# Kernel optimization log

Measured on AMD Instinct MI355X. Metric: run time of the kernel, lower is better.

Reference implementation:

```python
import jax, jax.numpy as jnp
import numpy as np

N_NODES = 50000
N_EDGES = 800000
D = 128
N_GRAPHS = 64


def setup_inputs() -> dict:
    key = jax.random.key(0)
    ks = jax.random.split(key, 9)
    x = jax.random.normal(ks[0], (N_NODES, D), dtype=jnp.float32)
    edge_index = jax.random.randint(ks[1], (2, N_EDGES), 0, N_NODES, dtype=jnp.int32)
    batch = jnp.sort(jax.random.randint(ks[2], (N_NODES,), 0, N_GRAPHS, dtype=jnp.int32))
    s = 1.0 / np.sqrt(D)
    W1 = jax.random.normal(ks[3], (D, D), jnp.float32) * s
    W2 = jax.random.normal(ks[4], (D, D), jnp.float32) * s
    W3 = jax.random.normal(ks[5], (D, D), jnp.float32) * s
    b1 = jnp.zeros((D,), jnp.float32)
    b2 = jnp.zeros((D,), jnp.float32)
    b3 = jnp.zeros((D,), jnp.float32)
    return {"x": x, "W1": W1, "b1": b1, "W2": W2, "b2": b2, "W3": W3, "b3": b3,
            "edge_index": edge_index, "batch": batch}


def _gcn_conv(x, W, b, src, dst, deg_inv_sqrt):
    # PyG GCNConv: x' = D^{-1/2} (A+I) D^{-1/2} (x W) + b
    h = x @ W                                    # [N, D]
    norm = (deg_inv_sqrt[src] * deg_inv_sqrt[dst])[:, None]   # [E, 1]
    agg = jax.ops.segment_sum(h[src] * norm, dst, num_segments=N_NODES)
    # self-loop contribution: norm_ii = deg_i^{-1}
    agg = agg + (deg_inv_sqrt * deg_inv_sqrt)[:, None] * h
    return agg + b


def reference(x, W1, b1, W2, b2, W3, b3, edge_index, batch):
    src, dst = edge_index[0], edge_index[1]
    # degree on A + I (self-loops added), edge weight 1
    deg = jax.ops.segment_sum(jnp.ones((N_EDGES,), x.dtype), dst,
                              num_segments=N_NODES) + 1.0
    deg_inv_sqrt = jax.lax.rsqrt(deg)
    h = jax.nn.relu(_gcn_conv(x, W1, b1, src, dst, deg_inv_sqrt))
    h = jax.nn.relu(_gcn_conv(h, W2, b2, src, dst, deg_inv_sqrt))
    h = _gcn_conv(h, W3, b3, src, dst, deg_inv_sqrt)
    # global_max_pool over graph ids
    return jax.ops.segment_max(h, batch, num_segments=N_GRAPHS)
```

## Files before the change

### kernel.cpp

```cpp
#include <hip/hip_runtime.h>
#include <float.h>
#include <math.h>

#define D 128
#define PCHUNK 64
#define NBUCK 256
#define BROWS 196
#define BCAP 4096
#define ACHUNK 3125

typedef _Float16 half8 __attribute__((ext_vector_type(8)));
typedef _Float16 half2v __attribute__((ext_vector_type(2)));
typedef float f32x4 __attribute__((ext_vector_type(4)));

__device__ __forceinline__ unsigned encf(float x) {
    unsigned u = __float_as_uint(x);
    return (u & 0x80000000u) ? ~u : (u | 0x80000000u);
}
__device__ __forceinline__ float decf(unsigned e) {
    unsigned u = (e & 0x80000000u) ? (e & 0x7FFFFFFFu) : ~e;
    return __uint_as_float(u);
}

__global__ __launch_bounds__(256) void binA_kernel(const int* __restrict__ src,
                                                   const int* __restrict__ dst,
                                                   int* __restrict__ gcnt,
                                                   uint2* __restrict__ gpair, int ne) {
    __shared__ int lh[NBUCK], ssc[NBUCK], lstart[NBUCK], gbase[NBUCK], loff[NBUCK];
    __shared__ uint2 stage[ACHUNK + 8];
    int t = threadIdx.x;
    int e0 = blockIdx.x * ACHUNK;
    int e1 = min(e0 + ACHUNK, ne);
    lh[t] = 0;
    __syncthreads();
    for (int e = e0 + t; e < e1; e += 256) atomicAdd(&lh[dst[e] / BROWS], 1);
    __syncthreads();
    ssc[t] = lh[t];
    __syncthreads();
    for (int off = 1; off < NBUCK; off <<= 1) {
        int u = (t >= off) ? ssc[t - off] : 0;
        __syncthreads();
        ssc[t] += u;
        __syncthreads();
    }
    int st = ssc[t] - lh[t];
    lstart[t] = st;
    loff[t] = st;
    if (lh[t] > 0) gbase[t] = atomicAdd(&gcnt[t], lh[t]);
    __syncthreads();
    for (int e = e0 + t; e < e1; e += 256) {
        int s = src[e], d = dst[e];
        int pos = atomicAdd(&loff[d / BROWS], 1);
        stage[pos] = make_uint2((unsigned)s, (unsigned)d);
    }
    __syncthreads();
    int m = e1 - e0;
    for (int i = t; i < m; i += 256) {
        uint2 pr = stage[i];
        int b = (int)pr.y / BROWS;
        int gpos = b * BCAP + gbase[b] + (i - lstart[b]);
        if (gpos < (b + 1) * BCAP) gpair[gpos] = pr;
    }
}

__global__ __launch_bounds__(256) void binB_kernel(const uint2* __restrict__ gpair,
                                                   const int* __restrict__ gcnt,
                                                   int* __restrict__ rowptr,
                                                   float* __restrict__ disv,
                                                   int* __restrict__ csr, int n) {
    __shared__ int lh[256], ssc[256], lstart[256], loff[256];
    __shared__ int gsc[NBUCK];
    __shared__ int cstage[BCAP];
    int b = blockIdx.x, t = threadIdx.x;
    int myc = gcnt[t];
    gsc[t] = myc;
    __syncthreads();
    for (int off = 1; off < NBUCK; off <<= 1) {
        int u = (t >= off) ? gsc[t - off] : 0;
        __syncthreads();
        gsc[t] += u;
        __syncthreads();
    }
    int bs = gsc[b] - gcnt[b];
    int m = min(gcnt[b], BCAP);
    int row0 = b * BROWS;
    int nrows = min(BROWS, n - row0);
    if (nrows <= 0) return;
    const uint2* mp = gpair + (size_t)b * BCAP;
    lh[t] = 0;
    __syncthreads();
    for (int i = t; i < m; i += 256) atomicAdd(&lh[(int)mp[i].y - row0], 1);
    __syncthreads();
    ssc[t] = lh[t];
    __syncthreads();
    for (int off = 1; off < 256; off <<= 1) {
        int u = (t >= off) ? ssc[t - off] : 0;
        __syncthreads();
        ssc[t] += u;
        __syncthreads();
    }
    int st = ssc[t] - lh[t];
    lstart[t] = st;
    loff[t] = st;
    __syncthreads();
    if (t <= nrows) rowptr[row0 + t] = bs + lstart[t];
    if (t < nrows) disv[row0 + t] = rsqrtf((float)lh[t] + 1.0f);
    for (int i = t; i < m; i += 256) {
        uint2 pr = mp[i];
        int pos = atomicAdd(&loff[(int)pr.y - row0], 1);
        cstage[pos] = (int)pr.x;
    }
    __syncthreads();
    for (int i = t; i < m; i += 256) csr[bs + i] = cstage[i];
}

__global__ void pack3_kernel(const float* __restrict__ W1, const float* __restrict__ W2,
                             const float* __restrict__ W3, _Float16* __restrict__ Wp1,
                             _Float16* __restrict__ Wp2, _Float16* __restrict__ Wp3,
                             unsigned* __restrict__ outEnc, int nout) {
    int gi = blockIdx.x * blockDim.x + threadIdx.x;
    if (gi < nout) outEnc[gi] = 0x007FFFFFu;
    int w = gi >> 14, i = gi & 16383;
    const float* W = (w == 0) ? W1 : (w == 1) ? W2 : W3;
    _Float16* Wp = (w == 0) ? Wp1 : (w == 1) ? Wp2 : Wp3;
    int j = i & 7, l = (i >> 3) & 63, t = (i >> 9) & 7, s = (i >> 12) & 3;
    int k = s * 32 + ((l >> 4) << 3) + j;
    int c = t * 16 + (l & 15);
    Wp[i] = (_Float16)W[k * 128 + c];
}

template <bool F32SRC>
__global__ __launch_bounds__(256) void gemm_mfma(const void* __restrict__ Xsrc,
                                                 const _Float16* __restrict__ Wp,
                                                 const float* __restrict__ disv,
                                                 _Float16* __restrict__ Gh,
                                                 int ntiles, int n) {
    __shared__ _Float16 Wl[16384];
    int tid = threadIdx.x;
    {
        const uint4* s4 = (const uint4*)Wp;
        uint4* d4 = (uint4*)Wl;
#pragma unroll
        for (int i = 0; i < 8; i++) d4[tid + 256 * i] = s4[tid + 256 * i];
    }
    __syncthreads();
    int wave = tid >> 6, lane = tid & 63;
    int m = lane & 15, quad = lane >> 4;
    const half8* wfrag = (const half8*)Wl;
    const _Float16* Xh = (const _Float16*)Xsrc;
    const float* Xf = (const float*)Xsrc;

    int tile = blockIdx.x * 4 + wave;
    if (tile >= ntiles) return;
    int arow = tile * 16 + m;
    if (arow >= n) arow = n - 1;

    f32x4 acc[8];
#pragma unroll
    for (int t = 0; t < 8; t++) acc[t] = (f32x4){0.f, 0.f, 0.f, 0.f};

#pragma unroll
    for (int s = 0; s < 4; s++) {
        half8 a;
        if (F32SRC) {
            float4 lo = *(const float4*)(Xf + (size_t)arow * D + s * 32 + quad * 8);
            float4 hi = *(const float4*)(Xf + (size_t)arow * D + s * 32 + quad * 8 + 4);
            a[0] = (_Float16)lo.x; a[1] = (_Float16)lo.y; a[2] = (_Float16)lo.z; a[3] = (_Float16)lo.w;
            a[4] = (_Float16)hi.x; a[5] = (_Float16)hi.y; a[6] = (_Float16)hi.z; a[7] = (_Float16)hi.w;
        } else {
            a = *(const half8*)(Xh + (size_t)arow * D + s * 32 + quad * 8);
        }
#pragma unroll
        for (int t = 0; t < 8; t++) {
            half8 b = wfrag[(s * 8 + t) * 64 + lane];
            acc[t] = __builtin_amdgcn_mfma_f32_16x16x32_f16(a, b, acc[t], 0, 0, 0);
        }
    }
    int orow0 = tile * 16 + quad * 4;
    if (orow0 + 3 < n) {
        float d0 = disv[orow0], d1 = disv[orow0 + 1], d2 = disv[orow0 + 2], d3 = disv[orow0 + 3];
#pragma unroll
        for (int t = 0; t < 8; t++) {
            int col = t * 16 + m;
            Gh[(size_t)(orow0 + 0) * D + col] = (_Float16)(acc[t][0] * d0);
            Gh[(size_t)(orow0 + 1) * D + col] = (_Float16)(acc[t][1] * d1);
            Gh[(size_t)(orow0 + 2) * D + col] = (_Float16)(acc[t][2] * d2);
            Gh[(size_t)(orow0 + 3) * D + col] = (_Float16)(acc[t][3] * d3);
        }
    } else {
#pragma unroll
        for (int t = 0; t < 8; t++) {
            int col = t * 16 + m;
#pragma unroll
            for (int r = 0; r < 4; r++) {
                int orow = orow0 + r;
                if (orow < n) Gh[(size_t)orow * D + col] = (_Float16)(acc[t][r] * disv[orow]);
            }
        }
    }
}

__global__ __launch_bounds__(256) void agg_f16(const _Float16* __restrict__ G,
                                               const int* __restrict__ rowptr,
                                               const int* __restrict__ csr,
                                               const float* __restrict__ disv,
                                               const float* __restrict__ bias,
                                               _Float16* __restrict__ Out, int n, int relu) {
    int wave = threadIdx.x >> 6, lane = threadIdx.x & 63;
    int node = blockIdx.x * 4 + wave;
    if (node >= n) return;
    int sub = lane >> 4, li = lane & 15;
    const half8* G8 = (const half8*)G;
    float acc[8];
    if (sub == 0) {
        half8 sv = G8[(size_t)node * 16 + li];
#pragma unroll
        for (int j = 0; j < 8; j++) acc[j] = (float)sv[j];
    } else {
#pragma unroll
        for (int j = 0; j < 8; j++) acc[j] = 0.f;
    }
    int e = rowptr[node], end = rowptr[node + 1];
    for (; e + 16 <= end; e += 16) {
        int i0 = csr[e + sub], i1 = csr[e + 4 + sub];
        int i2 = csr[e + 8 + sub], i3 = csr[e + 12 + sub];
        half8 v0 = G8[(size_t)i0 * 16 + li];
        half8 v1 = G8[(size_t)i1 * 16 + li];
        half8 v2 = G8[(size_t)i2 * 16 + li];
        half8 v3 = G8[(size_t)i3 * 16 + li];
#pragma unroll
        for (int j = 0; j < 8; j++)
            acc[j] += ((float)v0[j] + (float)v1[j]) + ((float)v2[j] + (float)v3[j]);
    }
    for (; e + 4 <= end; e += 4) {
        int i0 = csr[e + sub];
        half8 v0 = G8[(size_t)i0 * 16 + li];
#pragma unroll
        for (int j = 0; j < 8; j++) acc[j] += (float)v0[j];
    }
    int r = end - e;
    if (sub < r) {
        int i0 = csr[e + sub];
        half8 v0 = G8[(size_t)i0 * 16 + li];
#pragma unroll
        for (int j = 0; j < 8; j++) acc[j] += (float)v0[j];
    }
#pragma unroll
    for (int j = 0; j < 8; j++) {
        acc[j] += __shfl_xor(acc[j], 16);
        acc[j] += __shfl_xor(acc[j], 32);
    }
    if (sub == 0) {
        float dd = disv[node];
        float4 b0 = *(const float4*)&bias[li * 8];
        float4 b1 = *(const float4*)&bias[li * 8 + 4];
        float o0 = fmaf(dd, acc[0], b0.x), o1 = fmaf(dd, acc[1], b0.y);
        float o2 = fmaf(dd, acc[2], b0.z), o3 = fmaf(dd, acc[3], b0.w);
        float o4 = fmaf(dd, acc[4], b1.x), o5 = fmaf(dd, acc[5], b1.y);
        float o6 = fmaf(dd, acc[6], b1.z), o7 = fmaf(dd, acc[7], b1.w);
        if (relu) {
            o0 = fmaxf(o0, 0.f); o1 = fmaxf(o1, 0.f); o2 = fmaxf(o2, 0.f); o3 = fmaxf(o3, 0.f);
            o4 = fmaxf(o4, 0.f); o5 = fmaxf(o5, 0.f); o6 = fmaxf(o6, 0.f); o7 = fmaxf(o7, 0.f);
        }
        half8 h;
        h[0] = (_Float16)o0; h[1] = (_Float16)o1; h[2] = (_Float16)o2; h[3] = (_Float16)o3;
        h[4] = (_Float16)o4; h[5] = (_Float16)o5; h[6] = (_Float16)o6; h[7] = (_Float16)o7;
        ((half8*)Out)[(size_t)node * 16 + li] = h;
    }
}

__global__ __launch_bounds__(128) void pool_kernel(const _Float16* __restrict__ H,
                                                   const int* __restrict__ batch,
                                                   unsigned* __restrict__ outEnc, int n) {
    int half = threadIdx.x >> 6;
    int li = threadIdx.x & 63;
    int start = blockIdx.x * PCHUNK + half * (PCHUNK / 2);
    if (start >= n) return;
    int end = min(start + PCHUNK / 2, n);
    int c = li * 2;
    int curg = batch[start];
    float cx = -INFINITY, cy = -INFINITY;
    for (int i = start; i < end; i++) {
        half2v v = *(const half2v*)(H + (size_t)i * D + c);
        float vx = (float)v[0], vy = (float)v[1];
        int g = batch[i];
        if (g != curg) {
            atomicMax(&outEnc[curg * D + c], encf(cx));
            atomicMax(&outEnc[curg * D + c + 1], encf(cy));
            cx = vx; cy = vy; curg = g;
        } else {
            cx = fmaxf(cx, vx); cy = fmaxf(cy, vy);
        }
    }
    atomicMax(&outEnc[curg * D + c], encf(cx));
    atomicMax(&outEnc[curg * D + c + 1], encf(cy));
}

__global__ void decode_kernel(const unsigned* __restrict__ outEnc, float* __restrict__ out, int n) {
    int i = blockIdx.x * blockDim.x + threadIdx.x;
    if (i < n) out[i] = decf(outEnc[i]);
}

extern "C" void kernel_launch(void* const* d_in, const int* in_sizes, int n_in,
                              void* d_out, int out_size, void* d_ws, size_t ws_size,
                              hipStream_t stream) {
    const float* x  = (const float*)d_in[0];
    const float* W1 = (const float*)d_in[1];
    const float* b1 = (const float*)d_in[2];
    const float* W2 = (const float*)d_in[3];
    const float* b2 = (const float*)d_in[4];
    const float* W3 = (const float*)d_in[5];
    const float* b3 = (const float*)d_in[6];
    const int* ei    = (const int*)d_in[7];
    const int* batch = (const int*)d_in[8];

    int n  = in_sizes[0] / D;
    int ne = in_sizes[7] / 2;
    const int* src = ei;
    const int* dst = ei + ne;

    char* p = (char*)d_ws;
    auto alloc = [&](size_t bytes) -> void* {
        void* q = (void*)p;
        p += (bytes + 255) & ~(size_t)255;
        return q;
    };
    _Float16* Gh  = (_Float16*)alloc((size_t)n * D * 2);
    _Float16* Hh  = (_Float16*)alloc((size_t)n * D * 2);
    _Float16* Wp1 = (_Float16*)alloc((size_t)D * D * 2);
    _Float16* Wp2 = (_Float16*)alloc((size_t)D * D * 2);
    _Float16* Wp3 = (_Float16*)alloc((size_t)D * D * 2);
    int* gcnt     = (int*)alloc((size_t)NBUCK * 4);
    uint2* gpair  = (uint2*)alloc((size_t)NBUCK * BCAP * 8);
    int* rowptr   = (int*)alloc((size_t)(n + 1) * 4);
    int* csr      = (int*)alloc((size_t)ne * 4);
    float* disv   = (float*)alloc((size_t)n * 4);
    unsigned* outEnc = (unsigned*)alloc((size_t)out_size * 4);

    hipMemsetAsync(gcnt, 0, (size_t)NBUCK * 4, stream);

    int nblocksA = (ne + ACHUNK - 1) / ACHUNK;
    binA_kernel<<<nblocksA, 256, 0, stream>>>(src, dst, gcnt, gpair, ne);
    binB_kernel<<<NBUCK, 256, 0, stream>>>(gpair, gcnt, rowptr, disv, csr, n);
    pack3_kernel<<<192, 256, 0, stream>>>(W1, W2, W3, Wp1, Wp2, Wp3, outEnc, out_size);

    int ntiles = (n + 15) / 16;
    int gemm_blocks = (ntiles + 3) / 4;
    int agg_blocks  = (n + 3) / 4;

    gemm_mfma<true><<<gemm_blocks, 256, 0, stream>>>(x, Wp1, disv, Gh, ntiles, n);
    agg_f16<<<agg_blocks, 256, 0, stream>>>(Gh, rowptr, csr, disv, b1, Hh, n, 1);
    gemm_mfma<false><<<gemm_blocks, 256, 0, stream>>>(Hh, Wp2, disv, Gh, ntiles, n);
    agg_f16<<<agg_blocks, 256, 0, stream>>>(Gh, rowptr, csr, disv, b2, Hh, n, 1);
    gemm_mfma<false><<<gemm_blocks, 256, 0, stream>>>(Hh, Wp3, disv, Gh, ntiles, n);
    agg_f16<<<agg_blocks, 256, 0, stream>>>(Gh, rowptr, csr, disv, b3, Hh, n, 0);

    pool_kernel<<<(n + PCHUNK - 1) / PCHUNK, 128, 0, stream>>>(Hh, batch, outEnc, n);
    decode_kernel<<<(out_size + 255) / 256, 256, 0, stream>>>(outEnc, (float*)d_out, out_size);
}
```

Before: 259.1 us.

## Split features into 32-column chunks so the gather working set fits in cache

Stores the GEMM output and hidden features in a chunked layout of four 32-column planes, each [N,32]. Aggregation now runs one block group per chunk, with 4 nodes per wave and 4 edge streams per node. Each gather pass therefore only touches a 3.2MB plane, which should improve L2 hit rates for the random neighbour reads. The cost is that the CSR indices are read four times and each gather is a smaller 64B row segment. Index loads and output stores also become nontemporal.

```diff
diff --git a/kernel.cpp b/kernel.cpp
--- a/kernel.cpp
+++ b/kernel.cpp
@@ -3,6 +3,8 @@
 #include <math.h>
 
 #define D 128
+#define NCHUNK 4
+#define CHW 32
 #define PCHUNK 64
 #define NBUCK 256
 #define BROWS 196
@@ -168,7 +170,7 @@
             a[0] = (_Float16)lo.x; a[1] = (_Float16)lo.y; a[2] = (_Float16)lo.z; a[3] = (_Float16)lo.w;
             a[4] = (_Float16)hi.x; a[5] = (_Float16)hi.y; a[6] = (_Float16)hi.z; a[7] = (_Float16)hi.w;
         } else {
-            a = *(const half8*)(Xh + (size_t)arow * D + s * 32 + quad * 8);
+            a = *(const half8*)(Xh + ((size_t)s * n + arow) * CHW + quad * 8);
         }
 #pragma unroll
         for (int t = 0; t < 8; t++) {
@@ -181,79 +183,87 @@
         float d0 = disv[orow0], d1 = disv[orow0 + 1], d2 = disv[orow0 + 2], d3 = disv[orow0 + 3];
 #pragma unroll
         for (int t = 0; t < 8; t++) {
-            int col = t * 16 + m;
-            Gh[(size_t)(orow0 + 0) * D + col] = (_Float16)(acc[t][0] * d0);
-            Gh[(size_t)(orow0 + 1) * D + col] = (_Float16)(acc[t][1] * d1);
-            Gh[(size_t)(orow0 + 2) * D + col] = (_Float16)(acc[t][2] * d2);
-            Gh[(size_t)(orow0 + 3) * D + col] = (_Float16)(acc[t][3] * d3);
+            int col = (t & 1) * 16 + m;
+            size_t rb = (size_t)(t >> 1) * n;
+            Gh[(rb + orow0 + 0) * CHW + col] = (_Float16)(acc[t][0] * d0);
+            Gh[(rb + orow0 + 1) * CHW + col] = (_Float16)(acc[t][1] * d1);
+            Gh[(rb + orow0 + 2) * CHW + col] = (_Float16)(acc[t][2] * d2);
+            Gh[(rb + orow0 + 3) * CHW + col] = (_Float16)(acc[t][3] * d3);
         }
     } else {
 #pragma unroll
         for (int t = 0; t < 8; t++) {
-            int col = t * 16 + m;
+            int col = (t & 1) * 16 + m;
+            size_t rb = (size_t)(t >> 1) * n;
 #pragma unroll
             for (int r = 0; r < 4; r++) {
                 int orow = orow0 + r;
-                if (orow < n) Gh[(size_t)orow * D + col] = (_Float16)(acc[t][r] * disv[orow]);
+                if (orow < n) Gh[(rb + orow) * CHW + col] = (_Float16)(acc[t][r] * disv[orow]);
             }
         }
     }
 }
 
-__global__ __launch_bounds__(256) void agg_f16(const _Float16* __restrict__ G,
-                                               const int* __restrict__ rowptr,
-                                               const int* __restrict__ csr,
-                                               const float* __restrict__ disv,
-                                               const float* __restrict__ bias,
-                                               _Float16* __restrict__ Out, int n, int relu) {
+__global__ __launch_bounds__(256) void agg_chunk(const _Float16* __restrict__ G,
+                                                 const int* __restrict__ rowptr,
+                                                 const int* __restrict__ csr,
+                                                 const float* __restrict__ disv,
+                                                 const float* __restrict__ bias,
+                                                 _Float16* __restrict__ Out, int n, int relu,
+                                                 int nodeblocks) {
+    int chunk = blockIdx.x / nodeblocks;
+    int nb = blockIdx.x - chunk * nodeblocks;
     int wave = threadIdx.x >> 6, lane = threadIdx.x & 63;
-    int node = blockIdx.x * 4 + wave;
-    if (node >= n) return;
-    int sub = lane >> 4, li = lane & 15;
+    int node = nb * 16 + wave * 4 + (lane >> 4);
+    if (node >= n) node = n - 1;
+    int stream = (lane >> 2) & 3, li = lane & 3;
     const half8* G8 = (const half8*)G;
+    size_t cb4 = (size_t)chunk * n * 4;
+
     float acc[8];
-    if (sub == 0) {
-        half8 sv = G8[(size_t)node * 16 + li];
+    if (stream == 0) {
+        half8 sv = G8[cb4 + (size_t)node * 4 + li];
 #pragma unroll
         for (int j = 0; j < 8; j++) acc[j] = (float)sv[j];
     } else {
 #pragma unroll
         for (int j = 0; j < 8; j++) acc[j] = 0.f;
     }
-    int e = rowptr[node], end = rowptr[node + 1];
-    for (; e + 16 <= end; e += 16) {
-        int i0 = csr[e + sub], i1 = csr[e + 4 + sub];
-        int i2 = csr[e + 8 + sub], i3 = csr[e + 12 + sub];
-        half8 v0 = G8[(size_t)i0 * 16 + li];
-        half8 v1 = G8[(size_t)i1 * 16 + li];
-        half8 v2 = G8[(size_t)i2 * 16 + li];
-        half8 v3 = G8[(size_t)i3 * 16 + li];
-#pragma unroll
-        for (int j = 0; j < 8; j++)
-            acc[j] += ((float)v0[j] + (float)v1[j]) + ((float)v2[j] + (float)v3[j]);
-    }
-    for (; e + 4 <= end; e += 4) {
-        int i0 = csr[e + sub];
-        half8 v0 = G8[(size_t)i0 * 16 + li];
-#pragma unroll
-        for (int j = 0; j < 8; j++) acc[j] += (float)v0[j];
-    }
-    int r = end - e;
-    if (sub < r) {
-        int i0 = csr[e + sub];
-        half8 v0 = G8[(size_t)i0 * 16 + li];
-#pragma unroll
-        for (int j = 0; j < 8; j++) acc[j] += (float)v0[j];
+
+    int rs = rowptr[node], re = rowptr[node + 1];
+    for (int eb = rs + stream * 4; eb < re; eb += 16) {
+        int cnt = re - eb;
+        if (cnt >= 4) {
+            int i0 = __builtin_nontemporal_load(csr + eb);
+            int i1 = __builtin_nontemporal_load(csr + eb + 1);
+            int i2 = __builtin_nontemporal_load(csr + eb + 2);
+            int i3 = __builtin_nontemporal_load(csr + eb + 3);
+            half8 v0 = G8[cb4 + (size_t)i0 * 4 + li];
+            half8 v1 = G8[cb4 + (size_t)i1 * 4 + li];
+            half8 v2 = G8[cb4 + (size_t)i2 * 4 + li];
+            half8 v3 = G8[cb4 + (size_t)i3 * 4 + li];
+#pragma unroll
+            for (int j = 0; j < 8; j++)
+                acc[j] += ((float)v0[j] + (float)v1[j]) + ((float)v2[j] + (float)v3[j]);
+        } else {
+            for (int k = 0; k < cnt; k++) {
+                int i0 = __builtin_nontemporal_load(csr + eb + k);
+                half8 v = G8[cb4 + (size_t)i0 * 4 + li];
+#pragma unroll
+                for (int j = 0; j < 8; j++) acc[j] += (float)v[j];
+            }
+        }
     }
 #pragma unroll
     for (int j = 0; j < 8; j++) {
-        acc[j] += __shfl_xor(acc[j], 16);
-        acc[j] += __shfl_xor(acc[j], 32);
-    }
-    if (sub == 0) {
+        acc[j] += __shfl_xor(acc[j], 4);
+        acc[j] += __shfl_xor(acc[j], 8);
+    }
+    if (stream == 0) {
         float dd = disv[node];
-        float4 b0 = *(const float4*)&bias[li * 8];
-        float4 b1 = *(const float4*)&bias[li * 8 + 4];
+        int col0 = chunk * CHW + li * 8;
+        float4 b0 = *(const float4*)&bias[col0];
+        float4 b1 = *(const float4*)&bias[col0 + 4];
         float o0 = fmaf(dd, acc[0], b0.x), o1 = fmaf(dd, acc[1], b0.y);
         float o2 = fmaf(dd, acc[2], b0.z), o3 = fmaf(dd, acc[3], b0.w);
         float o4 = fmaf(dd, acc[4], b1.x), o5 = fmaf(dd, acc[5], b1.y);
@@ -265,7 +275,7 @@
         half8 h;
         h[0] = (_Float16)o0; h[1] = (_Float16)o1; h[2] = (_Float16)o2; h[3] = (_Float16)o3;
         h[4] = (_Float16)o4; h[5] = (_Float16)o5; h[6] = (_Float16)o6; h[7] = (_Float16)o7;
-        ((half8*)Out)[(size_t)node * 16 + li] = h;
+        __builtin_nontemporal_store(h, (half8*)Out + cb4 + (size_t)node * 4 + li);
     }
 }
 
@@ -278,10 +288,13 @@
     if (start >= n) return;
     int end = min(start + PCHUNK / 2, n);
     int c = li * 2;
+    int chnk = c >> 5;
+    int off = c & 31;
+    const _Float16* Hc = H + (size_t)chnk * n * CHW + off;
     int curg = batch[start];
     float cx = -INFINITY, cy = -INFINITY;
     for (int i = start; i < end; i++) {
-        half2v v = *(const half2v*)(H + (size_t)i * D + c);
+        half2v v = *(const half2v*)(Hc + (size_t)i * CHW);
         float vx = (float)v[0], vy = (float)v[1];
         int g = batch[i];
         if (g != curg) {
@@ -346,14 +359,15 @@
 
     int ntiles = (n + 15) / 16;
     int gemm_blocks = (ntiles + 3) / 4;
-    int agg_blocks  = (n + 3) / 4;
+    int nodeblocks = (n + 15) / 16;
+    int agg_blocks = NCHUNK * nodeblocks;
 
     gemm_mfma<true><<<gemm_blocks, 256, 0, stream>>>(x, Wp1, disv, Gh, ntiles, n);
-    agg_f16<<<agg_blocks, 256, 0, stream>>>(Gh, rowptr, csr, disv, b1, Hh, n, 1);
+    agg_chunk<<<agg_blocks, 256, 0, stream>>>(Gh, rowptr, csr, disv, b1, Hh, n, 1, nodeblocks);
     gemm_mfma<false><<<gemm_blocks, 256, 0, stream>>>(Hh, Wp2, disv, Gh, ntiles, n);
-    agg_f16<<<agg_blocks, 256, 0, stream>>>(Gh, rowptr, csr, disv, b2, Hh, n, 1);
+    agg_chunk<<<agg_blocks, 256, 0, stream>>>(Gh, rowptr, csr, disv, b2, Hh, n, 1, nodeblocks);
     gemm_mfma<false><<<gemm_blocks, 256, 0, stream>>>(Hh, Wp3, disv, Gh, ntiles, n);
-    agg_f16<<<agg_blocks, 256, 0, stream>>>(Gh, rowptr, csr, disv, b3, Hh, n, 0);
+    agg_chunk<<<agg_blocks, 256, 0, stream>>>(Gh, rowptr, csr, disv, b3, Hh, n, 0, nodeblocks);
 
     pool_kernel<<<(n + PCHUNK - 1) / PCHUNK, 128, 0, stream>>>(Hh, batch, outEnc, n);
     decode_kernel<<<(out_size + 255) / 256, 256, 0, stream>>>(outEnc, (float*)d_out, out_size);
```

After: 328.6 us. +26.8%, slower.

## Pad CSR rows to multiples of four with per-bucket layout and vectorized index loads

Applied to the files above, without the earlier changes.

binB now places each bucket's CSR segment at a fixed per-bucket offset, which drops the global prefix scan over bucket counts. Each row's neighbor list is padded to a multiple of four using self-indices, and rowptr becomes an (offset, degree) pair. The aggregation kernel removes the padding contribution by scaling the self term by (1 - npad). This lets it use int4/int2 vectorized index loads and a simpler tail with no partial-row branch. The GEMM kernel now handles two tiles per block. The cost is some extra gathers of padding entries and a larger CSR buffer.

```diff
diff --git a/kernel.cpp b/kernel.cpp
--- a/kernel.cpp
+++ b/kernel.cpp
@@ -7,6 +7,7 @@
 #define NBUCK 256
 #define BROWS 196
 #define BCAP 4096
+#define BCAPP 4896
 #define ACHUNK 3125
 
 typedef _Float16 half8 __attribute__((ext_vector_type(8)));
@@ -65,23 +66,12 @@
 
 __global__ __launch_bounds__(256) void binB_kernel(const uint2* __restrict__ gpair,
                                                    const int* __restrict__ gcnt,
-                                                   int* __restrict__ rowptr,
+                                                   int2* __restrict__ rowptr2,
                                                    float* __restrict__ disv,
                                                    int* __restrict__ csr, int n) {
-    __shared__ int lh[256], ssc[256], lstart[256], loff[256];
-    __shared__ int gsc[NBUCK];
-    __shared__ int cstage[BCAP];
+    __shared__ int lh[256], ssc[256], loff[256];
+    __shared__ int cstage[BCAPP];
     int b = blockIdx.x, t = threadIdx.x;
-    int myc = gcnt[t];
-    gsc[t] = myc;
-    __syncthreads();
-    for (int off = 1; off < NBUCK; off <<= 1) {
-        int u = (t >= off) ? gsc[t - off] : 0;
-        __syncthreads();
-        gsc[t] += u;
-        __syncthreads();
-    }
-    int bs = gsc[b] - gcnt[b];
     int m = min(gcnt[b], BCAP);
     int row0 = b * BROWS;
     int nrows = min(BROWS, n - row0);
@@ -91,7 +81,9 @@
     __syncthreads();
     for (int i = t; i < m; i += 256) atomicAdd(&lh[(int)mp[i].y - row0], 1);
     __syncthreads();
-    ssc[t] = lh[t];
+    int deg = lh[t];
+    int pdeg = (deg + 3) & ~3;
+    ssc[t] = pdeg;
     __syncthreads();
     for (int off = 1; off < 256; off <<= 1) {
         int u = (t >= off) ? ssc[t - off] : 0;
@@ -99,19 +91,25 @@
         ssc[t] += u;
         __syncthreads();
     }
-    int st = ssc[t] - lh[t];
-    lstart[t] = st;
+    int st = ssc[t] - pdeg;
     loff[t] = st;
     __syncthreads();
-    if (t <= nrows) rowptr[row0 + t] = bs + lstart[t];
-    if (t < nrows) disv[row0 + t] = rsqrtf((float)lh[t] + 1.0f);
+    int bbase = b * BCAPP;
+    if (t < nrows) {
+        rowptr2[row0 + t] = make_int2(bbase + st, deg);
+        disv[row0 + t] = rsqrtf((float)deg + 1.0f);
+    }
     for (int i = t; i < m; i += 256) {
         uint2 pr = mp[i];
         int pos = atomicAdd(&loff[(int)pr.y - row0], 1);
         cstage[pos] = (int)pr.x;
     }
-    __syncthreads();
-    for (int i = t; i < m; i += 256) csr[bs + i] = cstage[i];
+    if (t < nrows) {
+        for (int k = deg; k < pdeg; k++) cstage[st + k] = row0 + t;
+    }
+    __syncthreads();
+    int ptot = ssc[255];
+    for (int i = t; i < ptot; i += 256) csr[bbase + i] = cstage[i];
 }
 
 __global__ void pack3_kernel(const float* __restrict__ W1, const float* __restrict__ W2,
@@ -150,58 +148,61 @@
     const _Float16* Xh = (const _Float16*)Xsrc;
     const float* Xf = (const float*)Xsrc;
 
-    int tile = blockIdx.x * 4 + wave;
-    if (tile >= ntiles) return;
-    int arow = tile * 16 + m;
-    if (arow >= n) arow = n - 1;
-
-    f32x4 acc[8];
-#pragma unroll
-    for (int t = 0; t < 8; t++) acc[t] = (f32x4){0.f, 0.f, 0.f, 0.f};
-
-#pragma unroll
-    for (int s = 0; s < 4; s++) {
-        half8 a;
-        if (F32SRC) {
-            float4 lo = *(const float4*)(Xf + (size_t)arow * D + s * 32 + quad * 8);
-            float4 hi = *(const float4*)(Xf + (size_t)arow * D + s * 32 + quad * 8 + 4);
-            a[0] = (_Float16)lo.x; a[1] = (_Float16)lo.y; a[2] = (_Float16)lo.z; a[3] = (_Float16)lo.w;
-            a[4] = (_Float16)hi.x; a[5] = (_Float16)hi.y; a[6] = (_Float16)hi.z; a[7] = (_Float16)hi.w;
-        } else {
-            a = *(const half8*)(Xh + (size_t)arow * D + s * 32 + quad * 8);
-        }
-#pragma unroll
-        for (int t = 0; t < 8; t++) {
-            half8 b = wfrag[(s * 8 + t) * 64 + lane];
-            acc[t] = __builtin_amdgcn_mfma_f32_16x16x32_f16(a, b, acc[t], 0, 0, 0);
-        }
-    }
-    int orow0 = tile * 16 + quad * 4;
-    if (orow0 + 3 < n) {
-        float d0 = disv[orow0], d1 = disv[orow0 + 1], d2 = disv[orow0 + 2], d3 = disv[orow0 + 3];
-#pragma unroll
-        for (int t = 0; t < 8; t++) {
-            int col = t * 16 + m;
-            Gh[(size_t)(orow0 + 0) * D + col] = (_Float16)(acc[t][0] * d0);
-            Gh[(size_t)(orow0 + 1) * D + col] = (_Float16)(acc[t][1] * d1);
-            Gh[(size_t)(orow0 + 2) * D + col] = (_Float16)(acc[t][2] * d2);
-            Gh[(size_t)(orow0 + 3) * D + col] = (_Float16)(acc[t][3] * d3);
-        }
-    } else {
-#pragma unroll
-        for (int t = 0; t < 8; t++) {
-            int col = t * 16 + m;
-#pragma unroll
-            for (int r = 0; r < 4; r++) {
-                int orow = orow0 + r;
-                if (orow < n) Gh[(size_t)orow * D + col] = (_Float16)(acc[t][r] * disv[orow]);
+#pragma unroll
+    for (int pass = 0; pass < 2; pass++) {
+        int tile = blockIdx.x * 8 + pass * 4 + wave;
+        if (tile >= ntiles) continue;
+        int arow = tile * 16 + m;
+        if (arow >= n) arow = n - 1;
+
+        f32x4 acc[8];
+#pragma unroll
+        for (int t = 0; t < 8; t++) acc[t] = (f32x4){0.f, 0.f, 0.f, 0.f};
+
+#pragma unroll
+        for (int s = 0; s < 4; s++) {
+            half8 a;
+            if (F32SRC) {
+                float4 lo = *(const float4*)(Xf + (size_t)arow * D + s * 32 + quad * 8);
+                float4 hi = *(const float4*)(Xf + (size_t)arow * D + s * 32 + quad * 8 + 4);
+                a[0] = (_Float16)lo.x; a[1] = (_Float16)lo.y; a[2] = (_Float16)lo.z; a[3] = (_Float16)lo.w;
+                a[4] = (_Float16)hi.x; a[5] = (_Float16)hi.y; a[6] = (_Float16)hi.z; a[7] = (_Float16)hi.w;
+            } else {
+                a = *(const half8*)(Xh + (size_t)arow * D + s * 32 + quad * 8);
+            }
+#pragma unroll
+            for (int t = 0; t < 8; t++) {
+                half8 bf = wfrag[(s * 8 + t) * 64 + lane];
+                acc[t] = __builtin_amdgcn_mfma_f32_16x16x32_f16(a, bf, acc[t], 0, 0, 0);
             }
         }
+        int orow0 = tile * 16 + quad * 4;
+        if (orow0 + 3 < n) {
+            float d0 = disv[orow0], d1 = disv[orow0 + 1], d2 = disv[orow0 + 2], d3 = disv[orow0 + 3];
+#pragma unroll
+            for (int t = 0; t < 8; t++) {
+                int col = t * 16 + m;
+                Gh[(size_t)(orow0 + 0) * D + col] = (_Float16)(acc[t][0] * d0);
+                Gh[(size_t)(orow0 + 1) * D + col] = (_Float16)(acc[t][1] * d1);
+                Gh[(size_t)(orow0 + 2) * D + col] = (_Float16)(acc[t][2] * d2);
+                Gh[(size_t)(orow0 + 3) * D + col] = (_Float16)(acc[t][3] * d3);
+            }
+        } else {
+#pragma unroll
+            for (int t = 0; t < 8; t++) {
+                int col = t * 16 + m;
+#pragma unroll
+                for (int r = 0; r < 4; r++) {
+                    int orow = orow0 + r;
+                    if (orow < n) Gh[(size_t)orow * D + col] = (_Float16)(acc[t][r] * disv[orow]);
+                }
+            }
+        }
     }
 }
 
 __global__ __launch_bounds__(256) void agg_f16(const _Float16* __restrict__ G,
-                                               const int* __restrict__ rowptr,
+                                               const int2* __restrict__ rowptr2,
                                                const int* __restrict__ csr,
                                                const float* __restrict__ disv,
                                                const float* __restrict__ bias,
@@ -211,35 +212,40 @@
     if (node >= n) return;
     int sub = lane >> 4, li = lane & 15;
     const half8* G8 = (const half8*)G;
+    int2 rp = rowptr2[node];
+    int e0 = rp.x, deg = rp.y;
+    int pend = e0 + ((deg + 3) & ~3);
+    int npad = pend - e0 - deg;
     float acc[8];
     if (sub == 0) {
         half8 sv = G8[(size_t)node * 16 + li];
-#pragma unroll
-        for (int j = 0; j < 8; j++) acc[j] = (float)sv[j];
+        float w = (float)(1 - npad);
+#pragma unroll
+        for (int j = 0; j < 8; j++) acc[j] = w * (float)sv[j];
     } else {
 #pragma unroll
         for (int j = 0; j < 8; j++) acc[j] = 0.f;
     }
-    int e = rowptr[node], end = rowptr[node + 1];
-    for (; e + 16 <= end; e += 16) {
-        int i0 = csr[e + sub], i1 = csr[e + 4 + sub];
-        int i2 = csr[e + 8 + sub], i3 = csr[e + 12 + sub];
-        half8 v0 = G8[(size_t)i0 * 16 + li];
-        half8 v1 = G8[(size_t)i1 * 16 + li];
-        half8 v2 = G8[(size_t)i2 * 16 + li];
-        half8 v3 = G8[(size_t)i3 * 16 + li];
+    int e = e0;
+    for (; e + 16 <= pend; e += 16) {
+        int4 ix = *(const int4*)(csr + e + sub * 4);
+        half8 v0 = G8[(size_t)ix.x * 16 + li];
+        half8 v1 = G8[(size_t)ix.y * 16 + li];
+        half8 v2 = G8[(size_t)ix.z * 16 + li];
+        half8 v3 = G8[(size_t)ix.w * 16 + li];
 #pragma unroll
         for (int j = 0; j < 8; j++)
             acc[j] += ((float)v0[j] + (float)v1[j]) + ((float)v2[j] + (float)v3[j]);
     }
-    for (; e + 4 <= end; e += 4) {
-        int i0 = csr[e + sub];
-        half8 v0 = G8[(size_t)i0 * 16 + li];
-#pragma unroll
-        for (int j = 0; j < 8; j++) acc[j] += (float)v0[j];
-    }
-    int r = end - e;
-    if (sub < r) {
+    if (e + 8 <= pend) {
+        int2 ix = *(const int2*)(csr + e + sub * 2);
+        half8 v0 = G8[(size_t)ix.x * 16 + li];
+        half8 v1 = G8[(size_t)ix.y * 16 + li];
+#pragma unroll
+        for (int j = 0; j < 8; j++) acc[j] += (float)v0[j] + (float)v1[j];
+        e += 8;
+    }
+    if (e < pend) {
         int i0 = csr[e + sub];
         half8 v0 = G8[(size_t)i0 * 16 + li];
 #pragma unroll
@@ -332,8 +338,8 @@
     _Float16* Wp3 = (_Float16*)alloc((size_t)D * D * 2);
     int* gcnt     = (int*)alloc((size_t)NBUCK * 4);
     uint2* gpair  = (uint2*)alloc((size_t)NBUCK * BCAP * 8);
-    int* rowptr   = (int*)alloc((size_t)(n + 1) * 4);
-    int* csr      = (int*)alloc((size_t)ne * 4);
+    int2* rowptr2 = (int2*)alloc((size_t)n * 8);
+    int* csr      = (int*)alloc((size_t)NBUCK * BCAPP * 4);
     float* disv   = (float*)alloc((size_t)n * 4);
     unsigned* outEnc = (unsigned*)alloc((size_t)out_size * 4);
 
@@ -341,19 +347,19 @@
 
     int nblocksA = (ne + ACHUNK - 1) / ACHUNK;
     binA_kernel<<<nblocksA, 256, 0, stream>>>(src, dst, gcnt, gpair, ne);
-    binB_kernel<<<NBUCK, 256, 0, stream>>>(gpair, gcnt, rowptr, disv, csr, n);
+    binB_kernel<<<NBUCK, 256, 0, stream>>>(gpair, gcnt, rowptr2, disv, csr, n);
     pack3_kernel<<<192, 256, 0, stream>>>(W1, W2, W3, Wp1, Wp2, Wp3, outEnc, out_size);
 
     int ntiles = (n + 15) / 16;
-    int gemm_blocks = (ntiles + 3) / 4;
+    int gemm_blocks = (ntiles + 7) / 8;
     int agg_blocks  = (n + 3) / 4;
 
     gemm_mfma<true><<<gemm_blocks, 256, 0, stream>>>(x, Wp1, disv, Gh, ntiles, n);
-    agg_f16<<<agg_blocks, 256, 0, stream>>>(Gh, rowptr, csr, disv, b1, Hh, n, 1);
+    agg_f16<<<agg_blocks, 256, 0, stream>>>(Gh, rowptr2, csr, disv, b1, Hh, n, 1);
     gemm_mfma<false><<<gemm_blocks, 256, 0, stream>>>(Hh, Wp2, disv, Gh, ntiles, n);
-    agg_f16<<<agg_blocks, 256, 0, stream>>>(Gh, rowptr, csr, disv, b2, Hh, n, 1);
+    agg_f16<<<agg_blocks, 256, 0, stream>>>(Gh, rowptr2, csr, disv, b2, Hh, n, 1);
     gemm_mfma<false><<<gemm_blocks, 256, 0, stream>>>(Hh, Wp3, disv, Gh, ntiles, n);
-    agg_f16<<<agg_blocks, 256, 0, stream>>>(Gh, rowptr, csr, disv, b3, Hh, n, 0);
+    agg_f16<<<agg_blocks, 256, 0, stream>>>(Gh, rowptr2, csr, disv, b3, Hh, n, 0);
 
     pool_kernel<<<(n + PCHUNK - 1) / PCHUNK, 128, 0, stream>>>(Hh, batch, outEnc, n);
     decode_kernel<<<(out_size + 255) / 256, 256, 0, stream>>>(outEnc, (float*)d_out, out_size);
```

New measurement: 248.9 us. 3.9% less time.
